# Kernel optimization log

Hardware: AMD Instinct MI355X
Metric: run time of the kernel (lower is better)

Reference implementation:

```python
import jax, jax.numpy as jnp
import numpy as np

N, D_IN, D_OUT = 8192, 1024, 1024

def setup_inputs() -> dict:
    key = jax.random.key(0)
    k0, k1, k2, k3 = jax.random.split(key, 4)
    scale = 1.0 / np.sqrt(D_IN)
    return {
        "inputs": jax.random.normal(k0, (N, D_IN), dtype=jnp.float32),
        "W_q": jax.random.uniform(k1, (D_IN, D_OUT), jnp.float32, -scale, scale),
        "W_k": jax.random.uniform(k2, (D_IN, D_OUT), jnp.float32, -scale, scale),
        "W_v": jax.random.uniform(k3, (D_IN, D_OUT), jnp.float32, -scale, scale),
    }

def reference(inputs, W_q, W_k, W_v):
    # Linear projections (no bias): [N, d_out]
    q = inputs @ W_q
    k = inputs @ W_k
    v = inputs @ W_v
    d_k = k.shape[-1]
    # Full N x N scores, scaled softmax over last axis
    scores = (q @ k.T) / jnp.sqrt(jnp.asarray(d_k, q.dtype))
    attn = jax.nn.softmax(scores, axis=-1)
    return attn @ v
```

## Files before the change

kernel.cpp:

```cpp
#include <hip/hip_runtime.h>
#include <hip/hip_fp16.h>
#include <stdint.h>


typedef _Float16 half_t;
typedef _Float16 half8 __attribute__((ext_vector_type(8)));
typedef _Float16 half4 __attribute__((ext_vector_type(4)));
typedef float f32x4 __attribute__((ext_vector_type(4)));
typedef int i32x4 __attribute__((ext_vector_type(4)));

#define GLOAD16(gp, lp)                                                        \
  __builtin_amdgcn_global_load_lds(                                            \
      (__attribute__((address_space(1))) void*)(gp),                           \
      (__attribute__((address_space(3))) void*)(lp), 16, 0, 0)

#define BAR() __builtin_amdgcn_s_barrier()
#define VMCNT8() asm volatile("s_waitcnt vmcnt(8)")
#define VMCNT4() asm volatile("s_waitcnt vmcnt(4)")
#define VMCNT0() asm volatile("s_waitcnt vmcnt(0)")

__global__ __launch_bounds__(256) void cast_f32_to_f16(
    const float* __restrict__ in, half_t* __restrict__ out, int n4) {
  int i = blockIdx.x * 256 + threadIdx.x;
  if (i < n4) {
    float4 v = ((const float4*)in)[i];
    half4 o = {(half_t)v.x, (half_t)v.y, (half_t)v.z, (half_t)v.w};
    ((half4*)out)[i] = o;
  }
}

template <typename Tin>
__global__ __launch_bounds__(256) void transpose_cast(
    const Tin* __restrict__ in, int ldin, half_t* __restrict__ out, int ldout,
    int R, int C) {
  __shared__ half_t tile[64][65];
  const int c0 = blockIdx.x * 64, r0 = blockIdx.y * 64;
  const int tx = threadIdx.x & 63, ty = threadIdx.x >> 6;
#pragma unroll
  for (int i = 0; i < 16; i++) {
    int r = ty * 16 + i;
    tile[r][tx] = (half_t)in[(size_t)(r0 + r) * ldin + c0 + tx];
  }
  __syncthreads();
#pragma unroll
  for (int i = 0; i < 16; i++) {
    int c = ty * 16 + i;
    out[(size_t)(c0 + c) * ldout + r0 + tx] = tile[tx][c];
  }
}

__global__ __launch_bounds__(256) void rowsum_recip(
    const float* __restrict__ rowpart, float* __restrict__ rinv, int rows,
    int w4) {
  int r = blockIdx.x * 256 + threadIdx.x;
  if (r < rows) {
    const float4* p = (const float4*)(rowpart + (size_t)r * (w4 * 4));
    float s = 0.f;
    for (int i = 0; i < w4; i++) {
      float4 v = p[i];
      s += v.x + v.y + v.z + v.w;
    }
    rinv[r] = 1.f / s;
  }
}

__global__ __launch_bounds__(256) void reduce_add2h(
    const half8* __restrict__ a, const half8* __restrict__ b,
    float4* __restrict__ o, int n8) {
  int i = blockIdx.x * 256 + threadIdx.x;
  if (i < n8) {
    half8 x = a[i], y = b[i];
    float4 o0, o1;
    o0.x = (float)x[0] + (float)y[0];
    o0.y = (float)x[1] + (float)y[1];
    o0.z = (float)x[2] + (float)y[2];
    o0.w = (float)x[3] + (float)y[3];
    o1.x = (float)x[4] + (float)y[4];
    o1.y = (float)x[5] + (float)y[5];
    o1.z = (float)x[6] + (float)y[6];
    o1.w = (float)x[7] + (float)y[7];
    o[2 * i] = o0;
    o[2 * i + 1] = o1;
  }
}

template <typename To, int MODE>
__global__ __launch_bounds__(512, 2) void gemm256(
    const half_t* __restrict__ A, int lda, const half_t* __restrict__ Bt,
    int ldb, To* __restrict__ C, int ldc, int M, int N, int K, int ychunks,
    int SG, const float* __restrict__ rinv, int8_t* __restrict__ qi8,
    int8_t* __restrict__ ki8) {
  __shared__ __align__(16) char sm[131072];

  const int t = threadIdx.x;
  const int w = t >> 6;
  const int ln = t & 63;

  const int nwg = gridDim.x * gridDim.y;
  const int bid = blockIdx.y * gridDim.x + blockIdx.x;
  const int cpx = nwg >> 3;
  const int q = (bid & 7) * cpx + (bid >> 3);
  const int tiles_y = gridDim.y / ychunks;
  const int per_chunk = gridDim.x * tiles_y;
  const int chunk = q / per_chunk;
  int r_ = q - chunk * per_chunk;
  const int sw = SG * tiles_y;
  const int s_ = r_ / sw;
  r_ -= s_ * sw;
  const int by = r_ / SG;
  const int bx = s_ * SG + (r_ - by * SG);

  A += (size_t)chunk * K;
  Bt += (size_t)chunk * K;
  C += (size_t)chunk * M * ldc;

  const int row0 = by * 256;
  const int col0 = bx * 256;

  const int srow = w * 8 + (ln >> 3);
  const int sslot = (ln & 7) ^ ((ln >> 3) & 7);
  const half_t* Ag = A + (size_t)(row0 + srow) * lda + sslot * 8;
  const half_t* Bg = Bt + (size_t)(col0 + srow) * ldb + sslot * 8;
  const int ldsw = w * 1024;

#define STAGE_AB(kt, bb)                                                       \
  do {                                                                         \
    const half_t* ga_ = Ag + (size_t)(kt) * 64;                                \
    const half_t* gb_ = Bg + (size_t)(kt) * 64;                                \
    GLOAD16(ga_, sm + (bb) + ldsw);                                            \
    GLOAD16(ga_ + 64 * (size_t)lda, sm + (bb) + 8192 + ldsw);                  \
    GLOAD16(ga_ + 128 * (size_t)lda, sm + (bb) + 16384 + ldsw);                \
    GLOAD16(ga_ + 192 * (size_t)lda, sm + (bb) + 24576 + ldsw);                \
    GLOAD16(gb_, sm + (bb) + 32768 + ldsw);                                    \
    GLOAD16(gb_ + 64 * (size_t)ldb, sm + (bb) + 40960 + ldsw);                 \
    GLOAD16(gb_ + 128 * (size_t)ldb, sm + (bb) + 49152 + ldsw);                \
    GLOAD16(gb_ + 192 * (size_t)ldb, sm + (bb) + 57344 + ldsw);                \
  } while (0)

  const int wr = w >> 2;
  const int wc = w & 3;
  const int fr = ln & 15;
  const int kg = ln >> 4;
  const int sx0 = ((kg ^ (fr & 7)) << 4);
  const int sx1 = sx0 ^ 64;
  const int arow = (wr * 128 + fr) * 128;
  const int brow = 32768 + (wc * 64 + fr) * 128;

#define READ_A(MI0, cb)                                                        \
  _Pragma("unroll") for (int mi = 0; mi < 4; mi++) {                           \
    a4[mi][0] = *(const half8*)(sm + (cb) + arow + (MI0 + mi) * 2048 + sx0);   \
    a4[mi][1] = *(const half8*)(sm + (cb) + arow + (MI0 + mi) * 2048 + sx1);   \
  }
#define READ_B(NI, cb)                                                         \
  do {                                                                         \
    b8[NI][0] = *(const half8*)(sm + (cb) + brow + (NI) * 2048 + sx0);         \
    b8[NI][1] = *(const half8*)(sm + (cb) + brow + (NI) * 2048 + sx1);         \
  } while (0)

#define MFMA_Q(MI0, NI0)                                                       \
  __builtin_amdgcn_s_setprio(1);                                               \
  _Pragma("unroll") for (int kk = 0; kk < 2; kk++)                             \
  _Pragma("unroll") for (int mi = 0; mi < 4; mi++)                             \
  _Pragma("unroll") for (int ni = 0; ni < 2; ni++)                             \
      acc[MI0 + mi][NI0 + ni] = __builtin_amdgcn_mfma_f32_16x16x32_f16(        \
          a4[mi][kk], b8[NI0 + ni][kk], acc[MI0 + mi][NI0 + ni], 0, 0, 0);     \
  __builtin_amdgcn_s_setprio(0);

  half8 a4[4][2], b8[4][2];
  f32x4 acc[8][4] = {};

  const int NT = K >> 6;

  STAGE_AB(0, 0);
  STAGE_AB(1, 65536);
  VMCNT8();
  BAR();

#define TILE(tt, cb)                                                           \
  do {                                                                         \
    READ_A(0, cb);                                                             \
    READ_B(0, cb);                                                             \
    READ_B(1, cb);                                                             \
    BAR();                                                                     \
    MFMA_Q(0, 0);                                                              \
    BAR();                                                                     \
    READ_B(2, cb);                                                             \
    READ_B(3, cb);                                                             \
    BAR();                                                                     \
    MFMA_Q(0, 2);                                                              \
    BAR();                                                                     \
    READ_A(4, cb);                                                             \
    BAR();                                                                     \
    MFMA_Q(4, 2);                                                              \
    BAR();                                                                     \
    if ((tt) + 2 < NT) {                                                       \
      STAGE_AB((tt) + 2, cb);                                                  \
      VMCNT8();                                                                \
    } else {                                                                   \
      VMCNT0();                                                                \
    }                                                                          \
    BAR();                                                                     \
    MFMA_Q(4, 0);                                                              \
    BAR();                                                                     \
  } while (0)

  for (int kt = 0; kt < NT; kt += 2) {
    TILE(kt, 0);
    TILE(kt + 1, 65536);
  }

  const int orow = row0 + wr * 128 + (ln >> 4) * 4;
  const int ocol = col0 + wc * 64 + (ln & 15);
  if constexpr (MODE == 2) {
    if (bx < 8) {
      int8_t* qk = bx < 4 ? qi8 : ki8;
      const int cbase = ocol - (bx < 4 ? 0 : 1024);
#pragma unroll
      for (int mi = 0; mi < 8; mi++)
#pragma unroll
        for (int j = 0; j < 4; j++) {
          const size_t r = orow + mi * 16 + j;
#pragma unroll
          for (int ni = 0; ni < 4; ni++) {
            float f = acc[mi][ni][j] * 32.f;
            f = fminf(fmaxf(f, -127.f), 127.f);
            qk[r * 1024 + cbase + ni * 16] = (int8_t)rintf(f);
          }
        }
    } else {
#pragma unroll
      for (int mi = 0; mi < 8; mi++)
#pragma unroll
        for (int ni = 0; ni < 4; ni++) {
          const int c = ocol - 2048 + ni * 16;
          half4 v = {(half_t)acc[mi][ni][0], (half_t)acc[mi][ni][1],
                     (half_t)acc[mi][ni][2], (half_t)acc[mi][ni][3]};
          *(half4*)(C + (size_t)c * ldc + orow + mi * 16) = v;
        }
    }
  } else {
#pragma unroll
    for (int mi = 0; mi < 8; mi++)
#pragma unroll
      for (int ni = 0; ni < 4; ni++) {
        To* cp = C + (size_t)(orow + mi * 16) * ldc + ocol + ni * 16;
#pragma unroll
        for (int j = 0; j < 4; j++) cp[(size_t)j * ldc] = (To)acc[mi][ni][j];
      }
  }
#undef TILE
#undef MFMA_Q
#undef READ_A
#undef READ_B
#undef STAGE_AB
}

__global__ __launch_bounds__(512, 2) void gemm256_h32(
    const half_t* __restrict__ A, int lda, const half_t* __restrict__ Bt,
    int ldb, half_t* __restrict__ C, int ldc, int M, int K, int ychunks,
    int SG, const float* __restrict__ rinv) {
  __shared__ __align__(16) char sm[65536];

  const int t = threadIdx.x;
  const int w = t >> 6;
  const int ln = t & 63;

  const int nwg = gridDim.x * gridDim.y;
  const int bid = blockIdx.y * gridDim.x + blockIdx.x;
  const int cpx = nwg >> 3;
  const int q = (bid & 7) * cpx + (bid >> 3);
  const int tiles_y = gridDim.y / ychunks;
  const int per_chunk = gridDim.x * tiles_y;
  const int chunk = q / per_chunk;
  int r_ = q - chunk * per_chunk;
  const int sw = SG * tiles_y;
  const int s_ = r_ / sw;
  r_ -= s_ * sw;
  const int by = r_ / SG;
  const int bx = s_ * SG + (r_ - by * SG);

  A += (size_t)chunk * K;
  Bt += (size_t)chunk * K;
  C += (size_t)chunk * M * ldc;

  const int row0 = by * 256;
  const int col0 = bx * 256;

  const int rt = w * 16 + (ln >> 2);
  const int sl = (ln & 3) ^ ((rt >> 1) & 3);
  const half_t* Ag = A + (size_t)(row0 + rt) * lda + sl * 8;
  const half_t* Bg = Bt + (size_t)(col0 + rt) * ldb + sl * 8;
  const int ldsw = w * 1024;

#define STAGEH(kt, bb)                                                         \
  do {                                                                         \
    const half_t* ga_ = Ag + (size_t)(kt) * 32;                                \
    const half_t* gb_ = Bg + (size_t)(kt) * 32;                                \
    GLOAD16(ga_, sm + (bb) + ldsw);                                            \
    GLOAD16(ga_ + 128 * (size_t)lda, sm + (bb) + 8192 + ldsw);                 \
    GLOAD16(gb_, sm + (bb) + 16384 + ldsw);                                    \
    GLOAD16(gb_ + 128 * (size_t)ldb, sm + (bb) + 24576 + ldsw);                \
  } while (0)

  const int wr = w >> 2;
  const int wc = w & 3;
  const int fr = ln & 15;
  const int kg = ln >> 4;
  const int sx = (kg ^ ((fr >> 1) & 3)) << 4;
  const int arow = (wr * 128 + fr) * 64;
  const int brow = 16384 + (wc * 64 + fr) * 64;

#define RDH_A(MI0, cb)                                                         \
  _Pragma("unroll") for (int mi = 0; mi < 4; mi++)                             \
      ah[mi] = *(const half8*)(sm + (cb) + arow + ((MI0) + mi) * 1024 + sx);
#define RDH_B(NI, cb)                                                          \
  bh[NI] = *(const half8*)(sm + (cb) + brow + (NI) * 1024 + sx);

#define MMH_Q(MI0, NI0)                                                        \
  __builtin_amdgcn_s_setprio(1);                                               \
  _Pragma("unroll") for (int mi = 0; mi < 4; mi++)                             \
  _Pragma("unroll") for (int ni = 0; ni < 2; ni++)                             \
      acc[(MI0) + mi][(NI0) + ni] = __builtin_amdgcn_mfma_f32_16x16x32_f16(    \
          ah[mi], bh[(NI0) + ni], acc[(MI0) + mi][(NI0) + ni], 0, 0, 0);       \
  __builtin_amdgcn_s_setprio(0);

  half8 ah[4], bh[4];
  f32x4 acc[8][4] = {};

  const int NT = K >> 5;

  STAGEH(0, 0);
  STAGEH(1, 32768);
  VMCNT4();
  BAR();

#define TILEH(tt, cb)                                                          \
  do {                                                                         \
                                                                       \
    RDH_A(0, cb);                                                              \
    RDH_B(0, cb);                                                              \
    RDH_B(1, cb);                                                              \
    RDH_B(2, cb);                                                              \
    RDH_B(3, cb);                                                              \
    MMH_Q(0, 0);                                                               \
    MMH_Q(0, 2);                                                               \
                                                                       \
    RDH_A(4, cb);                                                              \
    MMH_Q(4, 2);                                                               \
    BAR();                    \
    if ((tt) + 2 < NT) {                                                       \
      STAGEH((tt) + 2, cb);                                                    \
      MMH_Q(4, 0);                                                             \
      VMCNT4();                     \
    } else {                                                                   \
      MMH_Q(4, 0);                                                             \
      VMCNT0();                                                                \
    }                                                                          \
    BAR();                                          \
  } while (0)

  for (int kt = 0; kt < NT; kt += 2) {
    TILEH(kt, 0);
    TILEH(kt + 1, 32768);
  }

  const int orow = row0 + wr * 128 + (ln >> 4) * 4;
  const int ocol = col0 + wc * 64 + (ln & 15);
#pragma unroll
  for (int mi = 0; mi < 8; mi++)
#pragma unroll
    for (int j = 0; j < 4; j++) {
      const size_t r = orow + mi * 16 + j;
      const float s = rinv[r];
#pragma unroll
      for (int ni = 0; ni < 4; ni++)
        C[r * ldc + ocol + ni * 16] = (half_t)(acc[mi][ni][j] * s);
    }
#undef TILEH
#undef MMH_Q
#undef RDH_A
#undef RDH_B
#undef STAGEH
}

__global__ __launch_bounds__(512, 2) void gemm256_i8exp(
    const int8_t* __restrict__ A, int lda, const int8_t* __restrict__ Bt,
    int ldb, half_t* __restrict__ C, int ldc, int K, int SG,
    float* __restrict__ rowpart) {
  __shared__ __align__(16) char sm[65536];

  const int t = threadIdx.x;
  const int w = t >> 6;
  const int ln = t & 63;

  const int nwg = gridDim.x * gridDim.y;
  const int bid = blockIdx.y * gridDim.x + blockIdx.x;
  const int cpx = nwg >> 3;
  const int q = (bid & 7) * cpx + (bid >> 3);
  const int sw = SG * gridDim.y;
  const int s_ = q / sw;
  int r_ = q - s_ * sw;
  const int by = r_ / SG;
  const int bx = s_ * SG + (r_ - by * SG);

  const int row0 = by * 256;
  const int col0 = bx * 256;

  const int rt = w * 16 + (ln >> 2);
  const int sl = (ln & 3) ^ ((rt >> 1) & 3);
  const int8_t* Ag = A + (size_t)(row0 + rt) * lda + sl * 16;
  const int8_t* Bg = Bt + (size_t)(col0 + rt) * ldb + sl * 16;
  const int ldsw = w * 1024;

#define STAGE8(kt, bb)                                                         \
  do {                                                                         \
    const int8_t* ga_ = Ag + (size_t)(kt) * 64;                                \
    const int8_t* gb_ = Bg + (size_t)(kt) * 64;                                \
    GLOAD16(ga_, sm + (bb) + ldsw);                                            \
    GLOAD16(ga_ + 128 * (size_t)lda, sm + (bb) + 8192 + ldsw);                 \
    GLOAD16(gb_, sm + (bb) + 16384 + ldsw);                                    \
    GLOAD16(gb_ + 128 * (size_t)ldb, sm + (bb) + 24576 + ldsw);                \
  } while (0)

  const int wr = w >> 2;
  const int wc = w & 3;
  const int fr = ln & 15;
  const int kg = ln >> 4;
  const int sx = (kg ^ ((fr >> 1) & 3)) << 4;
  const int arow = (wr * 128 + fr) * 64;
  const int brow = 16384 + (wc * 64 + fr) * 64;

#define READ_A8(MI0, cb)                                                       \
  _Pragma("unroll") for (int mi = 0; mi < 4; mi++)                             \
      a8[mi] = *(const i32x4*)(sm + (cb) + arow + (MI0 + mi) * 1024 + sx);
#define READ_B8(NI, cb)                                                        \
  b8v[NI] = *(const i32x4*)(sm + (cb) + brow + (NI) * 1024 + sx);

#define MFMA_Q8(MI0, NI0)                                                      \
  __builtin_amdgcn_s_setprio(1);                                               \
  _Pragma("unroll") for (int mi = 0; mi < 4; mi++)                             \
  _Pragma("unroll") for (int ni = 0; ni < 2; ni++)                             \
      acc[MI0 + mi][NI0 + ni] = __builtin_amdgcn_mfma_i32_16x16x64_i8(         \
          a8[mi], b8v[NI0 + ni], acc[MI0 + mi][NI0 + ni], 0, 0, 0);            \
  __builtin_amdgcn_s_setprio(0);

  i32x4 a8[4], b8v[4];
  i32x4 acc[8][4] = {};

  const int NT = K >> 6;

  STAGE8(0, 0);
  STAGE8(1, 32768);
  VMCNT4();
  BAR();

#define TILE8(tt, cb)                                                          \
  do {                                                                         \
                                                                       \
    READ_A8(0, cb);                                                            \
    READ_B8(0, cb);                                                            \
    READ_B8(1, cb);                                                            \
    READ_B8(2, cb);                                                            \
    READ_B8(3, cb);                                                            \
    MFMA_Q8(0, 0);                                                             \
    MFMA_Q8(0, 2);                                                             \
                                                                       \
    READ_A8(4, cb);                                                            \
    MFMA_Q8(4, 2);                                                             \
    BAR();        \
    if ((tt) + 2 < NT) {                                                       \
      STAGE8((tt) + 2, cb);                                                    \
      MFMA_Q8(4, 0);                                                           \
      VMCNT4();                     \
    } else {                                                                   \
      MFMA_Q8(4, 0);                                                           \
      VMCNT0();                                                                \
    }                                                                          \
    BAR();                             \
  } while (0)

  for (int kt = 0; kt < NT; kt += 2) {
    TILE8(kt, 0);
    TILE8(kt + 1, 32768);
  }

  const int orow = row0 + wr * 128 + (ln >> 4) * 4;
  const int ocol = col0 + wc * 64 + (ln & 15);
  const float sc = 3.0517578125e-5f;
  const int rp_ld = gridDim.x * 4;
#pragma unroll
  for (int mi = 0; mi < 8; mi++) {
#pragma unroll
    for (int j = 0; j < 4; j++) {
      const int r = orow + mi * 16 + j;
      float s = 0.f;
#pragma unroll
      for (int ni = 0; ni < 4; ni++) {
        float e = __expf((float)acc[mi][ni][j] * sc);
        C[(size_t)r * ldc + ocol + ni * 16] = (half_t)e;
        s += e;
      }
      s += __shfl_xor(s, 1);
      s += __shfl_xor(s, 2);
      s += __shfl_xor(s, 4);
      s += __shfl_xor(s, 8);
      if ((ln & 15) == 0) rowpart[(size_t)r * rp_ld + bx * 4 + wc] = s;
    }
  }
#undef TILE8
#undef MFMA_Q8
#undef READ_A8
#undef READ_B8
#undef STAGE8
}

extern "C" void kernel_launch(void* const* d_in, const int* in_sizes, int n_in,
                              void* d_out, int out_size, void* d_ws,
                              size_t ws_size, hipStream_t stream) {
  const float* X = (const float*)d_in[0];
  const float* Wq = (const float*)d_in[1];
  const float* Wk = (const float*)d_in[2];
  const float* Wv = (const float*)d_in[3];
  float* out = (float*)d_out;

  const int N = 8192, D = 1024;

  char* ws = (char*)d_ws;
  half_t* Xh   = (half_t*)(ws);
  half_t* Wth  = (half_t*)(ws + (16ull << 20));
  half_t* Vt   = (half_t*)(ws + (22ull << 20));
  half_t* partH= (half_t*)(ws + (38ull << 20));
  int8_t* Qi8  = (int8_t*)(ws + (70ull << 20));
  int8_t* Ki8  = (int8_t*)(ws + (78ull << 20));
  half_t* S    = (half_t*)(ws + (86ull << 20));
  float* rowpart = (float*)ws;
  float* rinv    = (float*)(ws + (4ull << 20));

  cast_f32_to_f16<<<(N * D / 4 + 255) / 256, 256, 0, stream>>>(X, Xh, N * D / 4);

  dim3 tg(D / 64, D / 64);
  transpose_cast<float><<<tg, 256, 0, stream>>>(Wq, D, Wth + 0ull * D * D, D, D, D);
  transpose_cast<float><<<tg, 256, 0, stream>>>(Wk, D, Wth + 1ull * D * D, D, D, D);
  transpose_cast<float><<<tg, 256, 0, stream>>>(Wv, D, Wth + 2ull * D * D, D, D, D);

  gemm256<half_t, 2><<<dim3(3 * D / 256, N / 256), 512, 0, stream>>>(
      Xh, D, Wth, D, Vt, N, N, 3 * D, D, 1, 4, nullptr, Qi8, Ki8);

  gemm256_i8exp<<<dim3(N / 256, N / 256), 512, 0, stream>>>(
      Qi8, D, Ki8, D, S, N, D, 8, rowpart);

  rowsum_recip<<<(N + 255) / 256, 256, 0, stream>>>(rowpart, rinv, N, 32);

  gemm256_h32<<<dim3(D / 256, 2 * N / 256), 512, 0, stream>>>(
      S, N, Vt, N, partH, D, N, N / 2, 2, 4, rinv);

  reduce_add2h<<<(N * D / 8 + 255) / 256, 256, 0, stream>>>(
      (const half8*)partH, (const half8*)(partH + (size_t)N * D), (float4*)out,
      N * D / 8);
}
```

Before: 320.1 us.

## Split attn@V GEMM into four K-chunks and reuse the pipelined kernel for projections

The attention-times-V GEMM now splits its K dimension into four chunks instead of two, doubling the grid to fill more compute units. Each chunk writes a partial fp16 result into its own buffer, and a four-way reduction kernel sums them. The QKV projection GEMM now uses the 64KB-LDS pipelined kernel body instead of the 128KB variant. This trades extra partial-output traffic and reduction work for better occupancy, and it places partial buffers in workspace regions that overlap Qi8 and rowpart data that is dead by then.

```diff
diff --git a/kernel.cpp b/kernel.cpp
--- a/kernel.cpp
+++ b/kernel.cpp
@@ -15,7 +15,6 @@
       (__attribute__((address_space(3))) void*)(lp), 16, 0, 0)
 
 #define BAR() __builtin_amdgcn_s_barrier()
-#define VMCNT8() asm volatile("s_waitcnt vmcnt(8)")
 #define VMCNT4() asm volatile("s_waitcnt vmcnt(4)")
 #define VMCNT0() asm volatile("s_waitcnt vmcnt(0)")
 
@@ -64,33 +63,35 @@
   }
 }
 
-__global__ __launch_bounds__(256) void reduce_add2h(
+__global__ __launch_bounds__(256) void reduce_add4h(
     const half8* __restrict__ a, const half8* __restrict__ b,
+    const half8* __restrict__ c, const half8* __restrict__ d,
     float4* __restrict__ o, int n8) {
   int i = blockIdx.x * 256 + threadIdx.x;
   if (i < n8) {
-    half8 x = a[i], y = b[i];
+    half8 x = a[i], y = b[i], z = c[i], u = d[i];
     float4 o0, o1;
-    o0.x = (float)x[0] + (float)y[0];
-    o0.y = (float)x[1] + (float)y[1];
-    o0.z = (float)x[2] + (float)y[2];
-    o0.w = (float)x[3] + (float)y[3];
-    o1.x = (float)x[4] + (float)y[4];
-    o1.y = (float)x[5] + (float)y[5];
-    o1.z = (float)x[6] + (float)y[6];
-    o1.w = (float)x[7] + (float)y[7];
+    o0.x = (float)x[0] + (float)y[0] + (float)z[0] + (float)u[0];
+    o0.y = (float)x[1] + (float)y[1] + (float)z[1] + (float)u[1];
+    o0.z = (float)x[2] + (float)y[2] + (float)z[2] + (float)u[2];
+    o0.w = (float)x[3] + (float)y[3] + (float)z[3] + (float)u[3];
+    o1.x = (float)x[4] + (float)y[4] + (float)z[4] + (float)u[4];
+    o1.y = (float)x[5] + (float)y[5] + (float)z[5] + (float)u[5];
+    o1.z = (float)x[6] + (float)y[6] + (float)z[6] + (float)u[6];
+    o1.w = (float)x[7] + (float)y[7] + (float)z[7] + (float)u[7];
     o[2 * i] = o0;
     o[2 * i + 1] = o1;
   }
 }
 
-template <typename To, int MODE>
-__global__ __launch_bounds__(512, 2) void gemm256(
+template <int MODE>
+__global__ __launch_bounds__(512, 2) void gemm256_h32(
     const half_t* __restrict__ A, int lda, const half_t* __restrict__ Bt,
-    int ldb, To* __restrict__ C, int ldc, int M, int N, int K, int ychunks,
-    int SG, const float* __restrict__ rinv, int8_t* __restrict__ qi8,
-    int8_t* __restrict__ ki8) {
-  __shared__ __align__(16) char sm[131072];
+    int ldb, half_t* __restrict__ C, int ldc, int K, int ychunks, int SG,
+    const float* __restrict__ rinv, int8_t* __restrict__ qi8,
+    int8_t* __restrict__ ki8, half_t* __restrict__ p1,
+    half_t* __restrict__ p2, half_t* __restrict__ p3) {
+  __shared__ __align__(16) char sm[65536];
 
   const int t = threadIdx.x;
   const int w = t >> 6;
@@ -112,176 +113,8 @@
 
   A += (size_t)chunk * K;
   Bt += (size_t)chunk * K;
-  C += (size_t)chunk * M * ldc;
-
-  const int row0 = by * 256;
-  const int col0 = bx * 256;
-
-  const int srow = w * 8 + (ln >> 3);
-  const int sslot = (ln & 7) ^ ((ln >> 3) & 7);
-  const half_t* Ag = A + (size_t)(row0 + srow) * lda + sslot * 8;
-  const half_t* Bg = Bt + (size_t)(col0 + srow) * ldb + sslot * 8;
-  const int ldsw = w * 1024;
-
-#define STAGE_AB(kt, bb)                                                       \
-  do {                                                                         \
-    const half_t* ga_ = Ag + (size_t)(kt) * 64;                                \
-    const half_t* gb_ = Bg + (size_t)(kt) * 64;                                \
-    GLOAD16(ga_, sm + (bb) + ldsw);                                            \
-    GLOAD16(ga_ + 64 * (size_t)lda, sm + (bb) + 8192 + ldsw);                  \
-    GLOAD16(ga_ + 128 * (size_t)lda, sm + (bb) + 16384 + ldsw);                \
-    GLOAD16(ga_ + 192 * (size_t)lda, sm + (bb) + 24576 + ldsw);                \
-    GLOAD16(gb_, sm + (bb) + 32768 + ldsw);                                    \
-    GLOAD16(gb_ + 64 * (size_t)ldb, sm + (bb) + 40960 + ldsw);                 \
-    GLOAD16(gb_ + 128 * (size_t)ldb, sm + (bb) + 49152 + ldsw);                \
-    GLOAD16(gb_ + 192 * (size_t)ldb, sm + (bb) + 57344 + ldsw);                \
-  } while (0)
-
-  const int wr = w >> 2;
-  const int wc = w & 3;
-  const int fr = ln & 15;
-  const int kg = ln >> 4;
-  const int sx0 = ((kg ^ (fr & 7)) << 4);
-  const int sx1 = sx0 ^ 64;
-  const int arow = (wr * 128 + fr) * 128;
-  const int brow = 32768 + (wc * 64 + fr) * 128;
-
-#define READ_A(MI0, cb)                                                        \
-  _Pragma("unroll") for (int mi = 0; mi < 4; mi++) {                           \
-    a4[mi][0] = *(const half8*)(sm + (cb) + arow + (MI0 + mi) * 2048 + sx0);   \
-    a4[mi][1] = *(const half8*)(sm + (cb) + arow + (MI0 + mi) * 2048 + sx1);   \
-  }
-#define READ_B(NI, cb)                                                         \
-  do {                                                                         \
-    b8[NI][0] = *(const half8*)(sm + (cb) + brow + (NI) * 2048 + sx0);         \
-    b8[NI][1] = *(const half8*)(sm + (cb) + brow + (NI) * 2048 + sx1);         \
-  } while (0)
-
-#define MFMA_Q(MI0, NI0)                                                       \
-  __builtin_amdgcn_s_setprio(1);                                               \
-  _Pragma("unroll") for (int kk = 0; kk < 2; kk++)                             \
-  _Pragma("unroll") for (int mi = 0; mi < 4; mi++)                             \
-  _Pragma("unroll") for (int ni = 0; ni < 2; ni++)                             \
-      acc[MI0 + mi][NI0 + ni] = __builtin_amdgcn_mfma_f32_16x16x32_f16(        \
-          a4[mi][kk], b8[NI0 + ni][kk], acc[MI0 + mi][NI0 + ni], 0, 0, 0);     \
-  __builtin_amdgcn_s_setprio(0);
-
-  half8 a4[4][2], b8[4][2];
-  f32x4 acc[8][4] = {};
-
-  const int NT = K >> 6;
-
-  STAGE_AB(0, 0);
-  STAGE_AB(1, 65536);
-  VMCNT8();
-  BAR();
-
-#define TILE(tt, cb)                                                           \
-  do {                                                                         \
-    READ_A(0, cb);                                                             \
-    READ_B(0, cb);                                                             \
-    READ_B(1, cb);                                                             \
-    BAR();                                                                     \
-    MFMA_Q(0, 0);                                                              \
-    BAR();                                                                     \
-    READ_B(2, cb);                                                             \
-    READ_B(3, cb);                                                             \
-    BAR();                                                                     \
-    MFMA_Q(0, 2);                                                              \
-    BAR();                                                                     \
-    READ_A(4, cb);                                                             \
-    BAR();                                                                     \
-    MFMA_Q(4, 2);                                                              \
-    BAR();                                                                     \
-    if ((tt) + 2 < NT) {                                                       \
-      STAGE_AB((tt) + 2, cb);                                                  \
-      VMCNT8();                                                                \
-    } else {                                                                   \
-      VMCNT0();                                                                \
-    }                                                                          \
-    BAR();                                                                     \
-    MFMA_Q(4, 0);                                                              \
-    BAR();                                                                     \
-  } while (0)
-
-  for (int kt = 0; kt < NT; kt += 2) {
-    TILE(kt, 0);
-    TILE(kt + 1, 65536);
-  }
-
-  const int orow = row0 + wr * 128 + (ln >> 4) * 4;
-  const int ocol = col0 + wc * 64 + (ln & 15);
-  if constexpr (MODE == 2) {
-    if (bx < 8) {
-      int8_t* qk = bx < 4 ? qi8 : ki8;
-      const int cbase = ocol - (bx < 4 ? 0 : 1024);
-#pragma unroll
-      for (int mi = 0; mi < 8; mi++)
-#pragma unroll
-        for (int j = 0; j < 4; j++) {
-          const size_t r = orow + mi * 16 + j;
-#pragma unroll
-          for (int ni = 0; ni < 4; ni++) {
-            float f = acc[mi][ni][j] * 32.f;
-            f = fminf(fmaxf(f, -127.f), 127.f);
-            qk[r * 1024 + cbase + ni * 16] = (int8_t)rintf(f);
-          }
-        }
-    } else {
-#pragma unroll
-      for (int mi = 0; mi < 8; mi++)
-#pragma unroll
-        for (int ni = 0; ni < 4; ni++) {
-          const int c = ocol - 2048 + ni * 16;
-          half4 v = {(half_t)acc[mi][ni][0], (half_t)acc[mi][ni][1],
-                     (half_t)acc[mi][ni][2], (half_t)acc[mi][ni][3]};
-          *(half4*)(C + (size_t)c * ldc + orow + mi * 16) = v;
-        }
-    }
-  } else {
-#pragma unroll
-    for (int mi = 0; mi < 8; mi++)
-#pragma unroll
-      for (int ni = 0; ni < 4; ni++) {
-        To* cp = C + (size_t)(orow + mi * 16) * ldc + ocol + ni * 16;
-#pragma unroll
-        for (int j = 0; j < 4; j++) cp[(size_t)j * ldc] = (To)acc[mi][ni][j];
-      }
-  }
-#undef TILE
-#undef MFMA_Q
-#undef READ_A
-#undef READ_B
-#undef STAGE_AB
-}
-
-__global__ __launch_bounds__(512, 2) void gemm256_h32(
-    const half_t* __restrict__ A, int lda, const half_t* __restrict__ Bt,
-    int ldb, half_t* __restrict__ C, int ldc, int M, int K, int ychunks,
-    int SG, const float* __restrict__ rinv) {
-  __shared__ __align__(16) char sm[65536];
-
-  const int t = threadIdx.x;
-  const int w = t >> 6;
-  const int ln = t & 63;
-
-  const int nwg = gridDim.x * gridDim.y;
-  const int bid = blockIdx.y * gridDim.x + blockIdx.x;
-  const int cpx = nwg >> 3;
-  const int q = (bid & 7) * cpx + (bid >> 3);
-  const int tiles_y = gridDim.y / ychunks;
-  const int per_chunk = gridDim.x * tiles_y;
-  const int chunk = q / per_chunk;
-  int r_ = q - chunk * per_chunk;
-  const int sw = SG * tiles_y;
-  const int s_ = r_ / sw;
-  r_ -= s_ * sw;
-  const int by = r_ / SG;
-  const int bx = s_ * SG + (r_ - by * SG);
-
-  A += (size_t)chunk * K;
-  Bt += (size_t)chunk * K;
-  C += (size_t)chunk * M * ldc;
+  if constexpr (MODE == 3)
+    C = chunk == 0 ? C : chunk == 1 ? p1 : chunk == 2 ? p2 : p3;
 
   const int row0 = by * 256;
   const int col0 = bx * 256;
@@ -366,16 +199,45 @@
 
   const int orow = row0 + wr * 128 + (ln >> 4) * 4;
   const int ocol = col0 + wc * 64 + (ln & 15);
-#pragma unroll
-  for (int mi = 0; mi < 8; mi++)
-#pragma unroll
-    for (int j = 0; j < 4; j++) {
-      const size_t r = orow + mi * 16 + j;
-      const float s = rinv[r];
-#pragma unroll
-      for (int ni = 0; ni < 4; ni++)
-        C[r * ldc + ocol + ni * 16] = (half_t)(acc[mi][ni][j] * s);
+  if constexpr (MODE == 2) {
+    if (bx < 8) {
+      int8_t* qk = bx < 4 ? qi8 : ki8;
+      const int cbase = ocol - (bx < 4 ? 0 : 1024);
+#pragma unroll
+      for (int mi = 0; mi < 8; mi++)
+#pragma unroll
+        for (int j = 0; j < 4; j++) {
+          const size_t r = orow + mi * 16 + j;
+#pragma unroll
+          for (int ni = 0; ni < 4; ni++) {
+            float f = acc[mi][ni][j] * 32.f;
+            f = fminf(fmaxf(f, -127.f), 127.f);
+            qk[r * 1024 + cbase + ni * 16] = (int8_t)rintf(f);
+          }
+        }
+    } else {
+#pragma unroll
+      for (int mi = 0; mi < 8; mi++)
+#pragma unroll
+        for (int ni = 0; ni < 4; ni++) {
+          const int c = ocol - 2048 + ni * 16;
+          half4 v = {(half_t)acc[mi][ni][0], (half_t)acc[mi][ni][1],
+                     (half_t)acc[mi][ni][2], (half_t)acc[mi][ni][3]};
+          *(half4*)(C + (size_t)c * ldc + orow + mi * 16) = v;
+        }
     }
+  } else {
+#pragma unroll
+    for (int mi = 0; mi < 8; mi++)
+#pragma unroll
+      for (int j = 0; j < 4; j++) {
+        const size_t r = orow + mi * 16 + j;
+        const float s = rinv[r];
+#pragma unroll
+        for (int ni = 0; ni < 4; ni++)
+          C[r * ldc + ocol + ni * 16] = (half_t)(acc[mi][ni][j] * s);
+      }
+  }
 #undef TILEH
 #undef MMH_Q
 #undef RDH_A
@@ -529,9 +391,12 @@
   half_t* Xh   = (half_t*)(ws);
   half_t* Wth  = (half_t*)(ws + (16ull << 20));
   half_t* Vt   = (half_t*)(ws + (22ull << 20));
-  half_t* partH= (half_t*)(ws + (38ull << 20));
+  half_t* P0   = (half_t*)(ws + (38ull << 20));
+  half_t* P1   = (half_t*)(ws + (54ull << 20));
   int8_t* Qi8  = (int8_t*)(ws + (70ull << 20));
   int8_t* Ki8  = (int8_t*)(ws + (78ull << 20));
+  half_t* P2   = (half_t*)(ws + (70ull << 20));
+  half_t* P3   = (half_t*)(ws + (6ull << 20));
   half_t* S    = (half_t*)(ws + (86ull << 20));
   float* rowpart = (float*)ws;
   float* rinv    = (float*)(ws + (4ull << 20));
@@ -543,18 +408,19 @@
   transpose_cast<float><<<tg, 256, 0, stream>>>(Wk, D, Wth + 1ull * D * D, D, D, D);
   transpose_cast<float><<<tg, 256, 0, stream>>>(Wv, D, Wth + 2ull * D * D, D, D, D);
 
-  gemm256<half_t, 2><<<dim3(3 * D / 256, N / 256), 512, 0, stream>>>(
-      Xh, D, Wth, D, Vt, N, N, 3 * D, D, 1, 4, nullptr, Qi8, Ki8);
+  gemm256_h32<2><<<dim3(3 * D / 256, N / 256), 512, 0, stream>>>(
+      Xh, D, Wth, D, Vt, N, D, 1, 4, nullptr, Qi8, Ki8, nullptr, nullptr,
+      nullptr);
 
   gemm256_i8exp<<<dim3(N / 256, N / 256), 512, 0, stream>>>(
       Qi8, D, Ki8, D, S, N, D, 8, rowpart);
 
   rowsum_recip<<<(N + 255) / 256, 256, 0, stream>>>(rowpart, rinv, N, 32);
 
-  gemm256_h32<<<dim3(D / 256, 2 * N / 256), 512, 0, stream>>>(
-      S, N, Vt, N, partH, D, N, N / 2, 2, 4, rinv);
-
-  reduce_add2h<<<(N * D / 8 + 255) / 256, 256, 0, stream>>>(
-      (const half8*)partH, (const half8*)(partH + (size_t)N * D), (float4*)out,
-      N * D / 8);
-}
+  gemm256_h32<3><<<dim3(D / 256, 4 * N / 256), 512, 0, stream>>>(
+      S, N, Vt, N, P0, D, N / 4, 4, 4, rinv, nullptr, nullptr, P1, P2, P3);
+
+  reduce_add4h<<<(N * D / 8 + 255) / 256, 256, 0, stream>>>(
+      (const half8*)P0, (const half8*)P1, (const half8*)P2, (const half8*)P3,
+      (float4*)out, N * D / 8);
+}
```

Result: slower. 327.0 us (+2.1%).
